# Optimization experiments

Measured on AMD Instinct MI355X. Metric: run time of the kernel, lower is better.

The kernel has to match this reference:

```python
import jax, jax.numpy as jnp
import numpy as np

D_MODEL = 1024
N_HEADS = 16
D_K = D_MODEL // N_HEADS
RANK = 16
LORA_SCALING = 32.0 / RANK  # alpha / rank = 2.0
LN_EPS = 1e-5


def _lora_linear(x, w, b, A, B):
    # torch nn.Linear: x @ w.T + b ; LoRA: (x @ A @ B) * scaling
    return x @ w.T + b + (x @ A @ B) * LORA_SCALING


def setup_inputs() -> dict:
    key = jax.random.key(0)
    ks = jax.random.split(key, 20)
    d = {}
    d['x'] = jax.random.normal(ks[0], (4, 1024, D_MODEL), dtype=jnp.float32)
    i = 1
    for p in ('q', 'k', 'v', 'o'):
        d[f'{p}_w'] = jax.random.normal(ks[i], (D_MODEL, D_MODEL), dtype=jnp.float32) * (1.0 / np.sqrt(D_MODEL)); i += 1
        d[f'{p}_b'] = jax.random.normal(ks[i], (D_MODEL,), dtype=jnp.float32) * 0.01; i += 1
        d[f'{p}_A'] = jax.random.normal(ks[i], (D_MODEL, RANK), dtype=jnp.float32) * 0.01; i += 1
        d[f'{p}_B'] = jax.random.normal(ks[i], (RANK, D_MODEL), dtype=jnp.float32) * 0.01; i += 1
    d['ln_g'] = jnp.ones((D_MODEL,), dtype=jnp.float32)
    d['ln_b'] = jnp.zeros((D_MODEL,), dtype=jnp.float32)
    return d


def reference(x, q_w, q_b, q_A, q_B, k_w, k_b, k_A, k_B,
              v_w, v_b, v_A, v_B, o_w, o_b, o_A, o_B, ln_g, ln_b):
    B, S, _ = x.shape
    # QKV projections with LoRA, reshape to [B, H, S, d_k]
    def split_heads(t):
        return t.reshape(B, S, N_HEADS, D_K).transpose(0, 2, 1, 3)
    Q = split_heads(_lora_linear(x, q_w, q_b, q_A, q_B))
    K = split_heads(_lora_linear(x, k_w, k_b, k_A, k_B))
    V = split_heads(_lora_linear(x, v_w, v_b, v_A, v_B))

    scores = jnp.einsum('bhqd,bhkd->bhqk', Q, K) / jnp.sqrt(jnp.float32(D_K))
    attn = jax.nn.softmax(scores, axis=-1)  # dropout is identity in eval
    ctx = jnp.einsum('bhqk,bhkd->bhqd', attn, V)
    ctx = ctx.transpose(0, 2, 1, 3).reshape(B, S, D_MODEL)

    out = _lora_linear(ctx, o_w, o_b, o_A, o_B)
    # residual + LayerNorm
    h = out + x
    mu = jnp.mean(h, axis=-1, keepdims=True)
    var = jnp.mean(jnp.square(h - mu), axis=-1, keepdims=True)
    normed = (h - mu) * jax.lax.rsqrt(var + LN_EPS) * ln_g + ln_b
    return normed, attn.mean(axis=1)
```

## Files before the change

### kernel.cpp

```cpp
#include <hip/hip_runtime.h>

#define DMODEL 1024
#define NHEADS 16
#define DHEAD  64
#define RANK   16
#define BATCH  4
#define SEQ    1024
#define MTOT   (BATCH*SEQ)
#define QSCALE 0.18033688011112042f

typedef __bf16 bf16;
typedef __bf16 bf16x8 __attribute__((ext_vector_type(8)));
typedef __bf16 bf16x4 __attribute__((ext_vector_type(4)));
typedef float  f32x4  __attribute__((ext_vector_type(4)));
typedef float  f32x16 __attribute__((ext_vector_type(16)));

__device__ __forceinline__ int swz128(int row, int byte_in_row) {
  int slot = byte_in_row >> 4;
  return row * 128 + (((slot ^ (row & 7)) << 4) | (byte_in_row & 15));
}

__device__ __forceinline__ void gll16(const void* g, void* l) {
  __builtin_amdgcn_global_load_lds((const __attribute__((address_space(1))) unsigned int*)g,
                                   (__attribute__((address_space(3))) unsigned int*)l, 16, 0, 0);
}

__device__ __forceinline__ unsigned pack2(float a, float b) {
  union { bf16 h[2]; unsigned u; } x;
  x.h[0] = (bf16)a; x.h[1] = (bf16)b;
  return x.u;
}

#define PSWAP(a, b) asm volatile("v_permlane32_swap_b32 %0, %1" : "+v"(a), "+v"(b));

#define TRRD(lo, hi, base, o0, o1)                                   \
  asm volatile("ds_read_b64_tr_b16 %0, %2 offset:" #o0 "\n\t"        \
               "ds_read_b64_tr_b16 %1, %2 offset:" #o1               \
               : "=v"(lo), "=v"(hi) : "v"(base));

__global__ void prep_kernel(
    const float* __restrict__ W0, const float* __restrict__ A0, const float* __restrict__ B0,
    const float* __restrict__ W1, const float* __restrict__ A1, const float* __restrict__ B1,
    const float* __restrict__ W2, const float* __restrict__ A2, const float* __restrict__ B2,
    const float* __restrict__ W3, const float* __restrict__ A3, const float* __restrict__ B3,
    bf16* __restrict__ out, const float* __restrict__ x, bf16* __restrict__ xb) {
  __shared__ float bsc[RANK];
  const int blk = blockIdx.x;
  if (blk < 4096) {
    const int l = blk >> 10;
    const float* W = l == 0 ? W0 : l == 1 ? W1 : l == 2 ? W2 : W3;
    const float* A = l == 0 ? A0 : l == 1 ? A1 : l == 2 ? A2 : A3;
    const float* Bm = l == 0 ? B0 : l == 1 ? B1 : l == 2 ? B2 : B3;
    bf16* o = out + (size_t)l * DMODEL * DMODEL;
    const int n = blk & 1023;
    if (threadIdx.x < RANK) bsc[threadIdx.x] = Bm[threadIdx.x * DMODEL + n] * 2.0f;
    __syncthreads();
    float br[RANK];
#pragma unroll
    for (int r = 0; r < RANK; ++r) br[r] = bsc[r];
    for (int k0 = 0; k0 < DMODEL; k0 += 256) {
      int k = k0 + threadIdx.x;
      float acc = W[n * DMODEL + k];
      const float4* arow = (const float4*)(A + k * RANK);
#pragma unroll
      for (int r4 = 0; r4 < 4; ++r4) {
        float4 a = arow[r4];
        acc += a.x*br[r4*4+0] + a.y*br[r4*4+1] + a.z*br[r4*4+2] + a.w*br[r4*4+3];
      }
      o[n * DMODEL + k] = (bf16)acc;
    }
  } else {
    int i = ((blk - 4096) * 256 + threadIdx.x) * 4;
    float4 v = *(const float4*)(x + i);
    bf16x4 o4 = { (bf16)v.x, (bf16)v.y, (bf16)v.z, (bf16)v.w };
    *(bf16x4*)(xb + i) = o4;
  }
}

__global__ __launch_bounds__(512) void gemm_qkv_kernel(
    const bf16* __restrict__ xb, const bf16* __restrict__ weff,
    const float* __restrict__ bq, const float* __restrict__ bk, const float* __restrict__ bv,
    bf16* __restrict__ Qb, bf16* __restrict__ Kb, bf16* __restrict__ Vb)
{
  __shared__ __align__(16) char sA[16384];
  __shared__ __align__(16) char sB[24576];
  const int tid = threadIdx.x, w = tid >> 6, lane = tid & 63;
  const int bid = blockIdx.x;
  const int nb = (bid & 7) * 64 + (bid >> 3);
  const int n0 = (nb & 15) * 192, m0 = (nb >> 4) * 128;
  const int wm = (w & 1) * 64, wn = (w >> 1) * 48;
  f32x4 acc[4][3] = {};

  const bf16* pA[2]; const bf16* pB[3]; char* lA[2]; char* lB[3];
#pragma unroll
  for (int i = 0; i < 2; ++i) {
    int ci = i * 8 + w;
    int row = ci * 8 + (lane >> 3);
    int ss = (lane & 7) ^ (row & 7);
    pA[i] = xb + (size_t)(m0 + row) * DMODEL + ss * 8;
    lA[i] = sA + ci * 1024;
  }
#pragma unroll
  for (int i = 0; i < 3; ++i) {
    int ci = i * 8 + w;
    int row = ci * 8 + (lane >> 3);
    int ss = (lane & 7) ^ (row & 7);
    pB[i] = weff + (size_t)(n0 + row) * DMODEL + ss * 8;
    lB[i] = sB + ci * 1024;
  }
  for (int kt = 0; kt < DMODEL / 64; ++kt) {
    const int kbase = kt * 64;
#pragma unroll
    for (int i = 0; i < 2; ++i) gll16(pA[i] + kbase, lA[i]);
#pragma unroll
    for (int i = 0; i < 3; ++i) gll16(pB[i] + kbase, lB[i]);
    __syncthreads();
#pragma unroll
    for (int ks = 0; ks < 2; ++ks) {
      bf16x8 af[4], bfg[3];
#pragma unroll
      for (int mi = 0; mi < 4; ++mi)
        af[mi] = *(const bf16x8*)(sA + swz128(wm + mi*16 + (lane & 15), ks*64 + (lane >> 4)*16));
#pragma unroll
      for (int ni = 0; ni < 3; ++ni)
        bfg[ni] = *(const bf16x8*)(sB + swz128(wn + ni*16 + (lane & 15), ks*64 + (lane >> 4)*16));
#pragma unroll
      for (int mi = 0; mi < 4; ++mi)
#pragma unroll
        for (int ni = 0; ni < 3; ++ni)
          acc[mi][ni] = __builtin_amdgcn_mfma_f32_16x16x32_bf16(af[mi], bfg[ni], acc[mi][ni], 0, 0, 0);
    }
    __syncthreads();
  }

#pragma unroll
  for (int mi = 0; mi < 4; ++mi) {
#pragma unroll
    for (int ni = 0; ni < 3; ++ni) {
      int col = n0 + wn + ni * 16 + (lane & 15);
      int zc = col >> 10;
      const float* bz = zc == 0 ? bq : (zc == 1 ? bk : bv);
      bf16* outp = zc == 0 ? Qb : (zc == 1 ? Kb : Vb);
      float scl = zc == 0 ? QSCALE : 1.0f;
      float bcol = bz[col & 1023];
      int h = (col >> 6) & 15, d = col & 63;
#pragma unroll
      for (int r = 0; r < 4; ++r) {
        int row = m0 + wm + mi * 16 + (lane >> 4) * 4 + r;
        float v = (acc[mi][ni][r] + bcol) * scl;
        int b = row >> 10, s = row & 1023;
        outp[(size_t)((b * NHEADS + h) * SEQ + s) * DHEAD + d] = (bf16)v;
      }
    }
  }
}

__global__ __launch_bounds__(256) void flash_kernel(
    const bf16* __restrict__ Qb, const bf16* __restrict__ Kb, const bf16* __restrict__ Vb,
    bf16* __restrict__ ctx, float* __restrict__ lstat)
{
  __shared__ __align__(16) char sK[2 * 8192];
  __shared__ __align__(16) char sV[2 * 8192];
  const int tid = threadIdx.x, w = tid >> 6, lane = tid & 63;
  const int l31 = lane & 31, lh = lane >> 5;
  const int bid = blockIdx.x;
  const int nb = (bid & 7) * 64 + (bid >> 3);
  const int bh = nb >> 3;
  const int q0 = (nb & 7) * 128;
  const bf16* Qbase = Qb + (size_t)bh * SEQ * DHEAD;
  const bf16* Kbase = Kb + (size_t)bh * SEQ * DHEAD;
  const bf16* Vbase = Vb + (size_t)bh * SEQ * DHEAD;
  const int qw = q0 + w * 32;

  bf16x8 aq[4];
#pragma unroll
  for (int kb = 0; kb < 4; ++kb)
    aq[kb] = *(const bf16x8*)(Qbase + (size_t)(qw + l31) * DHEAD + kb * 16 + lh * 8);

  const bf16* pK[2]; const bf16* pV[2]; int lKo[2], lVo[2];
#pragma unroll
  for (int i = 0; i < 2; ++i) {
    int ci = i * 4 + w;
    int rowK = ci * 8 + (lane >> 3);
    int ssK = (lane & 7) ^ (rowK & 7);
    pK[i] = Kbase + (size_t)rowK * DHEAD + ssK * 8;
    lKo[i] = ci * 1024;
    int kV = ci * 8 + ((lane >> 5) & 1) * 4 + ((lane >> 1) & 3);
    int dV = (((lane >> 3) & 3) << 4) + ((lane & 1) << 3);
    pV[i] = Vbase + (size_t)kV * DHEAD + dV;
    lVo[i] = ci * 1024;
  }

  const unsigned vb0 = (unsigned)(uintptr_t)sV + lh * 1024 + ((lane >> 4) & 1) * 128
                       + (lane & 15) * 8;

  f32x16 oacc[2] = {};
  float lsum = 0.f;

#pragma unroll
  for (int i = 0; i < 2; ++i) {
    gll16(pK[i], sK + lKo[i]);
    gll16(pV[i], sV + lVo[i]);
  }
  __syncthreads();

  for (int kt = 0; kt < SEQ / 64; ++kt) {
    const int cur = (kt & 1) << 13, nxt = cur ^ 8192;
    if (kt + 1 < SEQ / 64) {
      const size_t kofs = (size_t)(kt + 1) * 64 * DHEAD;
#pragma unroll
      for (int i = 0; i < 2; ++i) {
        gll16(pK[i] + kofs, sK + nxt + lKo[i]);
        gll16(pV[i] + kofs, sV + nxt + lVo[i]);
      }
    }

    f32x16 s[2] = {};
    __builtin_amdgcn_s_setprio(1);
#pragma unroll
    for (int ksb = 0; ksb < 2; ++ksb)
#pragma unroll
      for (int kb = 0; kb < 4; ++kb) {
        bf16x8 ak = *(const bf16x8*)(sK + cur + swz128(ksb*32 + l31, kb*32 + lh*16));
        s[ksb] = __builtin_amdgcn_mfma_f32_32x32x16_bf16(ak, aq[kb], s[ksb], 0, 0, 0);
      }
    __builtin_amdgcn_s_setprio(0);

    unsigned long long v0[4][2], v1[4][2];
    const unsigned vb = vb0 + cur;
    TRRD(v0[0][0], v1[0][0], vb, 0, 512)
    TRRD(v0[0][1], v1[0][1], vb, 256, 768)
    TRRD(v0[1][0], v1[1][0], vb, 2048, 2560)
    TRRD(v0[1][1], v1[1][1], vb, 2304, 2816)
    TRRD(v0[2][0], v1[2][0], vb, 4096, 4608)
    TRRD(v0[2][1], v1[2][1], vb, 4352, 4864)
    TRRD(v0[3][0], v1[3][0], vb, 6144, 6656)
    TRRD(v0[3][1], v1[3][1], vb, 6400, 6912)

    bf16x8 paf[4];
#pragma unroll
    for (int ksb = 0; ksb < 2; ++ksb) {
      float p[16];
#pragma unroll
      for (int r = 0; r < 16; ++r) {
        p[r] = __builtin_amdgcn_exp2f(s[ksb][r]);
        lsum += p[r];
      }
      unsigned a0 = pack2(p[0], p[1]),   b0 = pack2(p[4], p[5]);
      unsigned a1 = pack2(p[2], p[3]),   b1 = pack2(p[6], p[7]);
      PSWAP(a0, b0) PSWAP(a1, b1)
      unsigned c0 = pack2(p[8], p[9]),   d0 = pack2(p[12], p[13]);
      unsigned c1 = pack2(p[10], p[11]), d1 = pack2(p[14], p[15]);
      PSWAP(c0, d0) PSWAP(c1, d1)
      union { unsigned u[4]; bf16x8 v; } A0, A1;
      A0.u[0] = a0; A0.u[1] = a1; A0.u[2] = b0; A0.u[3] = b1;
      A1.u[0] = c0; A1.u[1] = c1; A1.u[2] = d0; A1.u[3] = d1;
      paf[ksb * 2 + 0] = A0.v;
      paf[ksb * 2 + 1] = A1.v;
    }

    asm volatile("s_waitcnt lgkmcnt(0)" ::: "memory");
    __builtin_amdgcn_sched_barrier(0);

    __builtin_amdgcn_s_setprio(1);
#pragma unroll
    for (int kbg = 0; kbg < 4; ++kbg)
#pragma unroll
      for (int db = 0; db < 2; ++db) {
        union { unsigned long long u[2]; bf16x8 v; } V;
        V.u[0] = v0[kbg][db]; V.u[1] = v1[kbg][db];
        oacc[db] = __builtin_amdgcn_mfma_f32_32x32x16_bf16(paf[kbg], V.v, oacc[db], 0, 0, 0);
      }
    __builtin_amdgcn_s_setprio(0);

    __syncthreads();
  }

  lsum += __shfl_xor(lsum, 32);
  float inv = __builtin_amdgcn_rcpf(lsum);

  const int b = bh >> 4, hh = bh & 15;
#pragma unroll
  for (int r = 0; r < 16; ++r) {
    int q_r = (r & 3) + 8 * (r >> 2) + 4 * lh;
    float sc = __shfl(inv, q_r);
    int row = qw + q_r;
#pragma unroll
    for (int db = 0; db < 2; ++db)
      ctx[(size_t)(b * SEQ + row) * DMODEL + hh * DHEAD + db * 32 + l31] =
          (bf16)(oacc[db][r] * sc);
  }
  if (lane < 32) lstat[(size_t)bh * SEQ + qw + lane] = lsum;
}

__global__ __launch_bounds__(256) void tail_kernel(
    const bf16* __restrict__ Qb, const bf16* __restrict__ Kb,
    const float* __restrict__ lstat, float* __restrict__ out2,
    const bf16* __restrict__ ctx, const bf16* __restrict__ weffo,
    const float* __restrict__ bias, const float* __restrict__ resid,
    float* __restrict__ outf)
{
  __shared__ __align__(16) char smem[2 * 16384];
  const int tid = threadIdx.x, w = tid >> 6, lane = tid & 63;

  if (blockIdx.x < 512) {
    char* sK = smem;
    const int bid = blockIdx.x;
    const int nb2 = (bid & 7) * 64 + (bid >> 3);
    const int b = nb2 >> 7;
    const int q0 = ((nb2 >> 3) & 15) * 64, k0 = (nb2 & 7) * 128;
    const int qw = q0 + w * 16;
    size_t goff[4]; int lofs[4];
#pragma unroll
    for (int i = 0; i < 4; ++i) {
      int chunk = i * 4 + w;
      int row = chunk * 8 + (lane >> 3);
      int ss = (lane & 7) ^ (row & 7);
      goff[i] = (size_t)(k0 + row) * DHEAD + ss * 8;
      lofs[i] = chunk * 1024;
    }
    const bf16* Kb_b = Kb + (size_t)b * NHEADS * SEQ * DHEAD;
    const bf16* Qb_b = Qb + (size_t)b * NHEADS * SEQ * DHEAD;

    f32x4 macc[8] = {};
#pragma unroll
    for (int i = 0; i < 4; ++i) gll16(Kb_b + goff[i], sK + lofs[i]);
    asm volatile("s_waitcnt vmcnt(0)" ::: "memory");
    __syncthreads();

    for (int h = 0; h < NHEADS; ++h) {
      const int cur = (h & 1) << 14, nxt = cur ^ 16384;
      if (h + 1 < NHEADS) {
        const bf16* Kn = Kb_b + (size_t)(h + 1) * SEQ * DHEAD;
#pragma unroll
        for (int i = 0; i < 4; ++i) gll16(Kn + goff[i], sK + nxt + lofs[i]);
      }
      const bf16* Qbase = Qb_b + (size_t)h * SEQ * DHEAD;
      bf16x8 aq[2];
#pragma unroll
      for (int ks = 0; ks < 2; ++ks)
        aq[ks] = *(const bf16x8*)(Qbase + (size_t)(qw + (lane & 15)) * DHEAD
                                  + ks * 32 + (lane >> 4) * 8);
      char* cK = sK + cur;
      f32x4 sc[8] = {};
#pragma unroll
      for (int ks = 0; ks < 2; ++ks)
#pragma unroll
        for (int ni = 0; ni < 8; ++ni) {
          bf16x8 bk = *(const bf16x8*)(cK + swz128(ni*16 + (lane & 15), ks*64 + (lane >> 4)*16));
          sc[ni] = __builtin_amdgcn_mfma_f32_16x16x32_bf16(aq[ks], bk, sc[ni], 0, 0, 0);
        }
      float lsc[4];
      const float* ls = lstat + ((size_t)(b * NHEADS + h)) * SEQ;
#pragma unroll
      for (int r = 0; r < 4; ++r)
        lsc[r] = 0.0625f * __builtin_amdgcn_rcpf(ls[qw + (lane >> 4)*4 + r]);
#pragma unroll
      for (int ni = 0; ni < 8; ++ni)
#pragma unroll
        for (int r = 0; r < 4; ++r)
          macc[ni][r] += __builtin_amdgcn_exp2f(sc[ni][r]) * lsc[r];
      asm volatile("s_waitcnt vmcnt(0)" ::: "memory");
      __syncthreads();
    }
#pragma unroll
    for (int r = 0; r < 4; ++r) {
      int qrow = qw + (lane >> 4) * 4 + r;
#pragma unroll
      for (int ni = 0; ni < 8; ++ni)
        out2[(size_t)(b * SEQ + qrow) * SEQ + k0 + ni * 16 + (lane & 15)] = macc[ni][r];
    }
  } else {
    char* sA = smem; char* sB = smem + 8192;
    const int bid = blockIdx.x - 512;
    const int nb = (bid & 7) * 64 + (bid >> 3);
    const int n0 = (nb & 7) * 128, m0 = (nb >> 3) * 64;
    const int wm = (w & 1) * 32, wn = (w >> 1) * 64;
    f32x4 acc[2][4] = {};
    const bf16* pA[2]; char* lA[2];
    const bf16* pB[4]; char* lB[4];
#pragma unroll
    for (int i = 0; i < 2; ++i) {
      int chunk = i * 4 + w;
      int row = chunk * 8 + (lane >> 3);
      int ss = (lane & 7) ^ (row & 7);
      pA[i] = ctx + (size_t)(m0 + row) * DMODEL + ss * 8;
      lA[i] = sA + chunk * 1024;
    }
#pragma unroll
    for (int i = 0; i < 4; ++i) {
      int chunk = i * 4 + w;
      int row = chunk * 8 + (lane >> 3);
      int ss = (lane & 7) ^ (row & 7);
      pB[i] = weffo + (size_t)(n0 + row) * DMODEL + ss * 8;
      lB[i] = sB + chunk * 1024;
    }
    for (int kt = 0; kt < DMODEL / 64; ++kt) {
      const int kbase = kt * 64;
#pragma unroll
      for (int i = 0; i < 2; ++i) gll16(pA[i] + kbase, lA[i]);
#pragma unroll
      for (int i = 0; i < 4; ++i) gll16(pB[i] + kbase, lB[i]);
      __syncthreads();
#pragma unroll
      for (int ks = 0; ks < 2; ++ks) {
        bf16x8 af[2], bfg[4];
#pragma unroll
        for (int mi = 0; mi < 2; ++mi)
          af[mi] = *(const bf16x8*)(sA + swz128(wm + mi*16 + (lane & 15), ks*64 + (lane >> 4)*16));
#pragma unroll
        for (int ni = 0; ni < 4; ++ni)
          bfg[ni] = *(const bf16x8*)(sB + swz128(wn + ni*16 + (lane & 15), ks*64 + (lane >> 4)*16));
#pragma unroll
        for (int mi = 0; mi < 2; ++mi)
#pragma unroll
          for (int ni = 0; ni < 4; ++ni)
            acc[mi][ni] = __builtin_amdgcn_mfma_f32_16x16x32_bf16(af[mi], bfg[ni], acc[mi][ni], 0, 0, 0);
      }
      __syncthreads();
    }
#pragma unroll
    for (int mi = 0; mi < 2; ++mi) {
#pragma unroll
      for (int ni = 0; ni < 4; ++ni) {
        int col = n0 + wn + ni * 16 + (lane & 15);
        float bcol = bias[col];
#pragma unroll
        for (int r = 0; r < 4; ++r) {
          int row = m0 + wm + mi * 16 + (lane >> 4) * 4 + r;
          outf[(size_t)row * DMODEL + col] =
              acc[mi][ni][r] + bcol + resid[(size_t)row * DMODEL + col];
        }
      }
    }
  }
}

__global__ __launch_bounds__(256) void ln_kernel(
    float* __restrict__ hb, const float* __restrict__ g,
    const float* __restrict__ bvec, float* __restrict__ out)
{
  const int row = blockIdx.x, t = threadIdx.x;
  float4 v = *(const float4*)(hb + (size_t)row * DMODEL + t * 4);
  float s = v.x + v.y + v.z + v.w;
  float s2 = v.x*v.x + v.y*v.y + v.z*v.z + v.w*v.w;
#pragma unroll
  for (int off = 32; off >= 1; off >>= 1) {
    s  += __shfl_down(s, off);
    s2 += __shfl_down(s2, off);
  }
  __shared__ float red[8];
  const int w = t >> 6;
  if ((t & 63) == 0) { red[w] = s; red[4 + w] = s2; }
  __syncthreads();
  if (t == 0) {
    red[0] = red[0] + red[1] + red[2] + red[3];
    red[4] = red[4] + red[5] + red[6] + red[7];
  }
  __syncthreads();
  float mu = red[0] * (1.0f / DMODEL);
  float var = red[4] * (1.0f / DMODEL) - mu * mu;
  float rs = rsqrtf(var + 1e-5f);
  float4 gv = *(const float4*)(g + t * 4);
  float4 bv = *(const float4*)(bvec + t * 4);
  float4 o;
  o.x = (v.x - mu) * rs * gv.x + bv.x;
  o.y = (v.y - mu) * rs * gv.y + bv.y;
  o.z = (v.z - mu) * rs * gv.z + bv.z;
  o.w = (v.w - mu) * rs * gv.w + bv.w;
  *(float4*)(out + (size_t)row * DMODEL + t * 4) = o;
}

extern "C" void kernel_launch(void* const* d_in, const int* in_sizes, int n_in,
                              void* d_out, int out_size, void* d_ws, size_t ws_size,
                              hipStream_t stream) {
  (void)in_sizes; (void)n_in; (void)out_size; (void)ws_size;
  const float* x = (const float*)d_in[0];
  const float* w_[4]  = {(const float*)d_in[1],  (const float*)d_in[5],
                         (const float*)d_in[9],  (const float*)d_in[13]};
  const float* b_[4]  = {(const float*)d_in[2],  (const float*)d_in[6],
                         (const float*)d_in[10], (const float*)d_in[14]};
  const float* A_[4]  = {(const float*)d_in[3],  (const float*)d_in[7],
                         (const float*)d_in[11], (const float*)d_in[15]};
  const float* Bm_[4] = {(const float*)d_in[4],  (const float*)d_in[8],
                         (const float*)d_in[12], (const float*)d_in[16]};
  const float* lng = (const float*)d_in[17];
  const float* lnb = (const float*)d_in[18];

  char* ws = (char*)d_ws;
  bf16* xb    = (bf16*)(ws);
  bf16* weff  = (bf16*)(ws + (8u  << 20));
  bf16* Qb    = (bf16*)(ws + (16u << 20));
  bf16* Kb    = (bf16*)(ws + (24u << 20));
  bf16* Vb    = (bf16*)(ws + (32u << 20));
  float* lstat = (float*)(ws + (40u << 20));
  bf16* ctx = xb;
  float* hbuf = (float*)d_out;
  float* out2 = (float*)d_out + (size_t)MTOT * DMODEL;

  prep_kernel<<<dim3(8192), dim3(256), 0, stream>>>(
      w_[0], A_[0], Bm_[0], w_[1], A_[1], Bm_[1],
      w_[2], A_[2], Bm_[2], w_[3], A_[3], Bm_[3], weff, x, xb);

  gemm_qkv_kernel<<<dim3(512), 512, 0, stream>>>(
      xb, weff, b_[0], b_[1], b_[2], Qb, Kb, Vb);

  flash_kernel<<<dim3(512), 256, 0, stream>>>(Qb, Kb, Vb, ctx, lstat);

  tail_kernel<<<dim3(1024), 256, 0, stream>>>(
      Qb, Kb, lstat, out2,
      ctx, weff + 3u * DMODEL * DMODEL, b_[3], x, hbuf);

  ln_kernel<<<dim3(MTOT), 256, 0, stream>>>(hbuf, lng, lnb, hbuf);
}
```

Baseline: 121.6 us.

## Use 128-key tiles in flash kernel and compute row sums via MFMA with ones

The flash attention kernel now stages 128 keys per iteration (double-buffered, 32KB each for K and V), processing two 64-key halves per barrier, which halves the number of __syncthreads and prefetch rounds. The per-lane scalar accumulation of exp values for the softmax denominator is replaced by an extra MFMA of the bf16 probabilities against a ones vector. This removes the VALU adds and the final cross-lane shuffles. The cost is one extra MFMA per k-block, bf16-rounded row sums, and doubled LDS use, which may lower occupancy.

```diff
diff --git a/kernel.cpp b/kernel.cpp
--- a/kernel.cpp
+++ b/kernel.cpp
@@ -159,8 +159,8 @@
     const bf16* __restrict__ Qb, const bf16* __restrict__ Kb, const bf16* __restrict__ Vb,
     bf16* __restrict__ ctx, float* __restrict__ lstat)
 {
-  __shared__ __align__(16) char sK[2 * 8192];
-  __shared__ __align__(16) char sV[2 * 8192];
+  __shared__ __align__(16) char sK[2 * 16384];
+  __shared__ __align__(16) char sV[2 * 16384];
   const int tid = threadIdx.x, w = tid >> 6, lane = tid & 63;
   const int l31 = lane & 31, lh = lane >> 5;
   const int bid = blockIdx.x;
@@ -177,120 +177,129 @@
   for (int kb = 0; kb < 4; ++kb)
     aq[kb] = *(const bf16x8*)(Qbase + (size_t)(qw + l31) * DHEAD + kb * 16 + lh * 8);
 
-  const bf16* pK[2]; const bf16* pV[2]; int lKo[2], lVo[2];
-#pragma unroll
-  for (int i = 0; i < 2; ++i) {
-    int ci = i * 4 + w;
-    int rowK = ci * 8 + (lane >> 3);
+  bf16x8 onesf;
+#pragma unroll
+  for (int j = 0; j < 8; ++j) onesf[j] = (bf16)1.0f;
+
+  const bf16* pK0; const bf16* pV0; int lKo0, lVo0;
+  {
+    int rowK = w * 8 + (lane >> 3);
     int ssK = (lane & 7) ^ (rowK & 7);
-    pK[i] = Kbase + (size_t)rowK * DHEAD + ssK * 8;
-    lKo[i] = ci * 1024;
-    int kV = ci * 8 + ((lane >> 5) & 1) * 4 + ((lane >> 1) & 3);
+    pK0 = Kbase + (size_t)rowK * DHEAD + ssK * 8;
+    lKo0 = w * 1024;
+    int kV = w * 8 + ((lane >> 5) & 1) * 4 + ((lane >> 1) & 3);
     int dV = (((lane >> 3) & 3) << 4) + ((lane & 1) << 3);
-    pV[i] = Vbase + (size_t)kV * DHEAD + dV;
-    lVo[i] = ci * 1024;
+    pV0 = Vbase + (size_t)kV * DHEAD + dV;
+    lVo0 = w * 1024;
   }
 
   const unsigned vb0 = (unsigned)(uintptr_t)sV + lh * 1024 + ((lane >> 4) & 1) * 128
                        + (lane & 15) * 8;
+  const unsigned kbase0 = (unsigned)(uintptr_t)sK;
 
   f32x16 oacc[2] = {};
-  float lsum = 0.f;
-
-#pragma unroll
-  for (int i = 0; i < 2; ++i) {
-    gll16(pK[i], sK + lKo[i]);
-    gll16(pV[i], sV + lVo[i]);
+  f32x16 lacc = {};
+
+#pragma unroll
+  for (int i = 0; i < 4; ++i) {
+    gll16(pK0 + (size_t)i * 32 * DHEAD, sK + lKo0 + i * 4096);
+    gll16(pV0 + (size_t)i * 32 * DHEAD, sV + lVo0 + i * 4096);
   }
   __syncthreads();
 
-  for (int kt = 0; kt < SEQ / 64; ++kt) {
-    const int cur = (kt & 1) << 13, nxt = cur ^ 8192;
-    if (kt + 1 < SEQ / 64) {
-      const size_t kofs = (size_t)(kt + 1) * 64 * DHEAD;
-#pragma unroll
-      for (int i = 0; i < 2; ++i) {
-        gll16(pK[i] + kofs, sK + nxt + lKo[i]);
-        gll16(pV[i] + kofs, sV + nxt + lVo[i]);
-      }
-    }
-
-    f32x16 s[2] = {};
-    __builtin_amdgcn_s_setprio(1);
-#pragma unroll
-    for (int ksb = 0; ksb < 2; ++ksb)
-#pragma unroll
-      for (int kb = 0; kb < 4; ++kb) {
-        bf16x8 ak = *(const bf16x8*)(sK + cur + swz128(ksb*32 + l31, kb*32 + lh*16));
-        s[ksb] = __builtin_amdgcn_mfma_f32_32x32x16_bf16(ak, aq[kb], s[ksb], 0, 0, 0);
-      }
-    __builtin_amdgcn_s_setprio(0);
-
-    unsigned long long v0[4][2], v1[4][2];
-    const unsigned vb = vb0 + cur;
-    TRRD(v0[0][0], v1[0][0], vb, 0, 512)
-    TRRD(v0[0][1], v1[0][1], vb, 256, 768)
-    TRRD(v0[1][0], v1[1][0], vb, 2048, 2560)
-    TRRD(v0[1][1], v1[1][1], vb, 2304, 2816)
-    TRRD(v0[2][0], v1[2][0], vb, 4096, 4608)
-    TRRD(v0[2][1], v1[2][1], vb, 4352, 4864)
-    TRRD(v0[3][0], v1[3][0], vb, 6144, 6656)
-    TRRD(v0[3][1], v1[3][1], vb, 6400, 6912)
-
-    bf16x8 paf[4];
-#pragma unroll
-    for (int ksb = 0; ksb < 2; ++ksb) {
-      float p[16];
-#pragma unroll
-      for (int r = 0; r < 16; ++r) {
-        p[r] = __builtin_amdgcn_exp2f(s[ksb][r]);
-        lsum += p[r];
-      }
-      unsigned a0 = pack2(p[0], p[1]),   b0 = pack2(p[4], p[5]);
-      unsigned a1 = pack2(p[2], p[3]),   b1 = pack2(p[6], p[7]);
-      PSWAP(a0, b0) PSWAP(a1, b1)
-      unsigned c0 = pack2(p[8], p[9]),   d0 = pack2(p[12], p[13]);
-      unsigned c1 = pack2(p[10], p[11]), d1 = pack2(p[14], p[15]);
-      PSWAP(c0, d0) PSWAP(c1, d1)
-      union { unsigned u[4]; bf16x8 v; } A0, A1;
-      A0.u[0] = a0; A0.u[1] = a1; A0.u[2] = b0; A0.u[3] = b1;
-      A1.u[0] = c0; A1.u[1] = c1; A1.u[2] = d0; A1.u[3] = d1;
-      paf[ksb * 2 + 0] = A0.v;
-      paf[ksb * 2 + 1] = A1.v;
-    }
-
-    asm volatile("s_waitcnt lgkmcnt(0)" ::: "memory");
-    __builtin_amdgcn_sched_barrier(0);
-
-    __builtin_amdgcn_s_setprio(1);
-#pragma unroll
-    for (int kbg = 0; kbg < 4; ++kbg)
-#pragma unroll
-      for (int db = 0; db < 2; ++db) {
-        union { unsigned long long u[2]; bf16x8 v; } V;
-        V.u[0] = v0[kbg][db]; V.u[1] = v1[kbg][db];
-        oacc[db] = __builtin_amdgcn_mfma_f32_32x32x16_bf16(paf[kbg], V.v, oacc[db], 0, 0, 0);
-      }
-    __builtin_amdgcn_s_setprio(0);
-
+  for (int kt = 0; kt < SEQ / 128; ++kt) {
+    const int cur = (kt & 1) << 14, nxt = cur ^ 16384;
+    if (kt + 1 < SEQ / 128) {
+      const size_t kofs = (size_t)(kt + 1) * 128 * DHEAD;
+#pragma unroll
+      for (int i = 0; i < 4; ++i) {
+        gll16(pK0 + kofs + (size_t)i * 32 * DHEAD, sK + nxt + lKo0 + i * 4096);
+        gll16(pV0 + kofs + (size_t)i * 32 * DHEAD, sV + nxt + lVo0 + i * 4096);
+      }
+    }
+
+#pragma unroll
+    for (int half = 0; half < 2; ++half) {
+      const int hb_ = cur + half * 8192;
+      f32x16 s[2] = {};
+      __builtin_amdgcn_s_setprio(1);
+#pragma unroll
+      for (int ksb = 0; ksb < 2; ++ksb)
+#pragma unroll
+        for (int kb = 0; kb < 4; ++kb) {
+          bf16x8 ak = *(const bf16x8*)(sK + hb_ + swz128(ksb*32 + l31, kb*32 + lh*16));
+          s[ksb] = __builtin_amdgcn_mfma_f32_32x32x16_bf16(ak, aq[kb], s[ksb], 0, 0, 0);
+        }
+      __builtin_amdgcn_s_setprio(0);
+
+      unsigned long long v0[4][2], v1[4][2];
+      const unsigned vb = vb0 + hb_;
+      TRRD(v0[0][0], v1[0][0], vb, 0, 512)
+      TRRD(v0[0][1], v1[0][1], vb, 256, 768)
+      TRRD(v0[1][0], v1[1][0], vb, 2048, 2560)
+      TRRD(v0[1][1], v1[1][1], vb, 2304, 2816)
+      TRRD(v0[2][0], v1[2][0], vb, 4096, 4608)
+      TRRD(v0[2][1], v1[2][1], vb, 4352, 4864)
+      TRRD(v0[3][0], v1[3][0], vb, 6144, 6656)
+      TRRD(v0[3][1], v1[3][1], vb, 6400, 6912)
+
+      bf16x8 paf[4];
+#pragma unroll
+      for (int ksb = 0; ksb < 2; ++ksb) {
+        float p[16];
+#pragma unroll
+        for (int r = 0; r < 16; ++r)
+          p[r] = __builtin_amdgcn_exp2f(s[ksb][r]);
+        unsigned a0 = pack2(p[0], p[1]),   b0 = pack2(p[4], p[5]);
+        unsigned a1 = pack2(p[2], p[3]),   b1 = pack2(p[6], p[7]);
+        PSWAP(a0, b0) PSWAP(a1, b1)
+        unsigned c0 = pack2(p[8], p[9]),   d0 = pack2(p[12], p[13]);
+        unsigned c1 = pack2(p[10], p[11]), d1 = pack2(p[14], p[15]);
+        PSWAP(c0, d0) PSWAP(c1, d1)
+        union { unsigned u[4]; bf16x8 v; } A0, A1;
+        A0.u[0] = a0; A0.u[1] = a1; A0.u[2] = b0; A0.u[3] = b1;
+        A1.u[0] = c0; A1.u[1] = c1; A1.u[2] = d0; A1.u[3] = d1;
+        paf[ksb * 2 + 0] = A0.v;
+        paf[ksb * 2 + 1] = A1.v;
+      }
+
+      asm volatile("s_waitcnt lgkmcnt(0)" ::: "memory");
+      __builtin_amdgcn_sched_barrier(0);
+
+      __builtin_amdgcn_s_setprio(1);
+#pragma unroll
+      for (int kbg = 0; kbg < 4; ++kbg) {
+#pragma unroll
+        for (int db = 0; db < 2; ++db) {
+          union { unsigned long long u[2]; bf16x8 v; } V;
+          V.u[0] = v0[kbg][db]; V.u[1] = v1[kbg][db];
+          oacc[db] = __builtin_amdgcn_mfma_f32_32x32x16_bf16(paf[kbg], V.v, oacc[db], 0, 0, 0);
+        }
+        lacc = __builtin_amdgcn_mfma_f32_32x32x16_bf16(paf[kbg], onesf, lacc, 0, 0, 0);
+      }
+      __builtin_amdgcn_s_setprio(0);
+    }
     __syncthreads();
   }
-
-  lsum += __shfl_xor(lsum, 32);
-  float inv = __builtin_amdgcn_rcpf(lsum);
 
   const int b = bh >> 4, hh = bh & 15;
 #pragma unroll
   for (int r = 0; r < 16; ++r) {
     int q_r = (r & 3) + 8 * (r >> 2) + 4 * lh;
-    float sc = __shfl(inv, q_r);
+    float inv = __builtin_amdgcn_rcpf(lacc[r]);
     int row = qw + q_r;
 #pragma unroll
     for (int db = 0; db < 2; ++db)
       ctx[(size_t)(b * SEQ + row) * DMODEL + hh * DHEAD + db * 32 + l31] =
-          (bf16)(oacc[db][r] * sc);
-  }
-  if (lane < 32) lstat[(size_t)bh * SEQ + qw + lane] = lsum;
+          (bf16)(oacc[db][r] * inv);
+  }
+  if (l31 == 0) {
+#pragma unroll
+    for (int r = 0; r < 16; ++r) {
+      int q_r = (r & 3) + 8 * (r >> 2) + 4 * lh;
+      lstat[(size_t)bh * SEQ + qw + q_r] = lacc[r];
+    }
+  }
 }
 
 __global__ __launch_bounds__(256) void tail_kernel(
```

Result: no change. 120.4 us (-1.0%).
